# Kernel tuning notes

Measured on AMD Instinct MI355X. Metric: run time of the kernel, lower is better.

The kernel has to match this reference:

```python
import jax, jax.numpy as jnp
import numpy as np

N_NODES = 100000
BN_EPS = 1e-5


def _linear_params(key, fan_in, fan_out):
    k1, k2 = jax.random.split(key)
    lim = 1.0 / np.sqrt(fan_in)
    W = jax.random.uniform(k1, (fan_in, fan_out), jnp.float32, -lim, lim)
    b = jax.random.uniform(k2, (fan_out,), jnp.float32, -lim, lim)
    return W, b


def setup_inputs() -> dict:
    key = jax.random.key(0)
    ks = jax.random.split(key, 24)
    in_ch, hid, tdim, L = 17, 64, 32, 2
    E = 1600000
    inp = {}
    inp["x"] = jax.random.normal(ks[0], (N_NODES, in_ch), jnp.float32)
    inp["edge_index"] = jax.random.randint(ks[1], (2, E), 0, N_NODES, jnp.int64)
    inp["edge_dts"] = jax.random.uniform(ks[2], (E,), jnp.float32) * 100.0
    inp["batch_size"] = 10000
    # TimeEncode params (learned, TGAT init)
    inp["basis_freq"] = jnp.asarray(1.0 / 10 ** np.linspace(0, 9, tdim), jnp.float32)
    inp["phase"] = jnp.zeros((tdim,), jnp.float32)
    # TMP edge MLP: in = 2*in_ch + tdim
    mi = 2 * in_ch + tdim
    inp["tmp_W1"], inp["tmp_b1"] = _linear_params(ks[3], mi, mi // 2)
    inp["tmp_W2"], inp["tmp_b2"] = _linear_params(ks[4], mi // 2, in_ch)
    inp["proj_W"], inp["proj_b"] = _linear_params(ks[5], in_ch, hid)
    # SMP layers (stacked over L)
    si = 2 * hid
    W1s, b1s, W2s, b2s = [], [], [], []
    for l in range(L):
        W1, b1 = _linear_params(ks[6 + 2 * l], si, si // 2)
        W2, b2 = _linear_params(ks[7 + 2 * l], si // 2, hid)
        W1s.append(W1); b1s.append(b1); W2s.append(W2); b2s.append(b2)
    inp["smp_W1"] = jnp.stack(W1s); inp["smp_b1"] = jnp.stack(b1s)
    inp["smp_W2"] = jnp.stack(W2s); inp["smp_b2"] = jnp.stack(b2s)
    inp["bn_gamma"] = jnp.ones((L, hid), jnp.float32)
    inp["bn_beta"] = jnp.zeros((L, hid), jnp.float32)
    # classifier head
    inp["clf_W1"], inp["clf_b1"] = _linear_params(ks[12], hid, hid)
    inp["clf_g1"] = jnp.ones((hid,), jnp.float32); inp["clf_bb1"] = jnp.zeros((hid,), jnp.float32)
    inp["clf_W2"], inp["clf_b2"] = _linear_params(ks[13], hid, hid // 2)
    inp["clf_g2"] = jnp.ones((hid // 2,), jnp.float32); inp["clf_bb2"] = jnp.zeros((hid // 2,), jnp.float32)
    inp["clf_W3"], inp["clf_b3"] = _linear_params(ks[14], hid // 2, 1)
    return inp


def _segment_mean(vals, idx, n):
    s = jax.ops.segment_sum(vals, idx, num_segments=n)
    c = jax.ops.segment_sum(jnp.ones((idx.shape[0], 1), vals.dtype), idx, num_segments=n)
    return s / jnp.maximum(c, 1.0)


def _bn(x, g, b):
    m = x.mean(0)
    v = x.var(0)
    return (x - m) * jax.lax.rsqrt(v + BN_EPS) * g + b


def reference(x, edge_index, edge_dts, batch_size, basis_freq, phase,
              tmp_W1, tmp_b1, tmp_W2, tmp_b2, proj_W, proj_b,
              smp_W1, smp_b1, smp_W2, smp_b2, bn_gamma, bn_beta,
              clf_W1, clf_b1, clf_g1, clf_bb1,
              clf_W2, clf_b2, clf_g2, clf_bb2, clf_W3, clf_b3):
    src, dst = edge_index[0], edge_index[1]  # x_j = x[src], x_i = x[dst]
    n = x.shape[0]
    # TimeEncode: cos(t * freq + phase)  -> [E, time_dim]
    rel = jnp.cos(edge_dts[:, None] * basis_freq + phase)
    # --- TMP conv (applied once) ---
    x_i = x[dst]
    m_in = jnp.concatenate([x_i, x[src], rel], axis=-1)
    p = jnp.tanh(jax.nn.relu(m_in @ tmp_W1 + tmp_b1) @ tmp_W2 + tmp_b2)
    msg = (2.0 * p - 1.0) * x_i  # (p - q) * x_i with q = 1 - p
    h = x + _segment_mean(msg, dst, n)
    # --- project to hidden ---
    h = h @ proj_W + proj_b
    # --- L SMP layers with BatchNorm + ReLU (dropout = eval/identity) ---
    L = smp_W1.shape[0]
    for l in range(L):
        h_i = h[dst]
        m_in = jnp.concatenate([h_i, h[src]], axis=-1)
        p = jnp.tanh(jax.nn.relu(m_in @ smp_W1[l] + smp_b1[l]) @ smp_W2[l] + smp_b2[l])
        h = h + _segment_mean((2.0 * p - 1.0) * h_i, dst, n)
        h = jax.nn.relu(_bn(h, bn_gamma[l], bn_beta[l]))
    # --- classifier on seed nodes ---
    z = h[:batch_size]
    z = jax.nn.relu(_bn(z @ clf_W1 + clf_b1, clf_g1, clf_bb1))
    z = jax.nn.relu(_bn(z @ clf_W2 + clf_b2, clf_g2, clf_bb2))
    return z @ clf_W3 + clf_b3  # [batch_size, 1] logits
```

## Files before the change

### kernel.cpp

```cpp
#include <hip/hip_runtime.h>
#include <hip/hip_bf16.h>


typedef float  f32x4 __attribute__((ext_vector_type(4)));
typedef short  s16x8 __attribute__((ext_vector_type(8)));

__device__ __forceinline__ float tanh_factor(float u) {
  float e = __expf(2.0f * u);
  return fmaf(-4.0f, __builtin_amdgcn_rcpf(e + 1.0f), 1.0f);
}

__device__ __forceinline__ void atomic_add_f32(float* p, float v) {
  unsafeAtomicAdd(p, v);
}

__device__ __forceinline__ unsigned short f2bf(float f) {
  __hip_bfloat16 b = __float2bfloat16(f);
  return *(unsigned short*)&b;
}
__device__ __forceinline__ float bf2f(unsigned short u) {
  unsigned int v = ((unsigned int)u) << 16;
  return *(float*)&v;
}

__global__ __launch_bounds__(256) void k_hist(
    const int* __restrict__ ei, int* __restrict__ cntI, int E)
{
  int e = blockIdx.x * 256 + threadIdx.x;
  if (e < E) atomicAdd(&cntI[__builtin_nontemporal_load(ei + E + e)], 1);
}

__global__ __launch_bounds__(256) void k_scan_block(
    const int* __restrict__ cntI, int* __restrict__ cursor,
    int* __restrict__ bsum, int N)
{
  __shared__ int s[256];
  const int t = threadIdx.x;
  int i = blockIdx.x * 256 + t;
  int v = (i < N) ? cntI[i] : 0;
  s[t] = v;
  for (int off = 1; off < 256; off <<= 1) {
    __syncthreads();
    int x = (t >= off) ? s[t - off] : 0;
    __syncthreads();
    s[t] += x;
  }
  __syncthreads();
  if (i < N) cursor[i] = s[t] - v;
  if (t == 255) bsum[blockIdx.x] = s[255];
}

__global__ __launch_bounds__(512) void k_scan_bsum(int* __restrict__ bsum, int nb)
{
  __shared__ int s[512];
  const int t = threadIdx.x;
  int v = (t < nb) ? bsum[t] : 0;
  s[t] = v;
  for (int off = 1; off < 512; off <<= 1) {
    __syncthreads();
    int x = (t >= off) ? s[t - off] : 0;
    __syncthreads();
    s[t] += x;
  }
  __syncthreads();
  if (t < nb) bsum[t] = s[t] - v;
}

__global__ __launch_bounds__(256) void k_expand_add(
    int* __restrict__ cursor, const int* __restrict__ bsum,
    const int* __restrict__ cntI, int* __restrict__ dstS, int N)
{
  int n = blockIdx.x * 256 + threadIdx.x;
  if (n >= N) return;
  int cur = cursor[n] + bsum[blockIdx.x];
  cursor[n] = cur;
  int c = cntI[n];
  for (int i = 0; i < c; i++) dstS[cur + i] = n;
}

__global__ __launch_bounds__(256) void k_scatter_x(
    const int* __restrict__ ei, const float* __restrict__ dts,
    int* __restrict__ cursor, int2* __restrict__ srcdtS, int E, int N)
{
  const int g  = blockIdx.x & 7;
  const int bi = blockIdx.x >> 3;
  const int nb = gridDim.x >> 3;
  const int lo = (int)(((long long)N * g) >> 3);
  const int hi = (int)(((long long)N * (g + 1)) >> 3);
  for (int e = bi * 256 + threadIdx.x; e < E; e += nb * 256) {
    int d = __builtin_nontemporal_load(ei + E + e);
    if (d >= lo && d < hi) {
      int s = __builtin_nontemporal_load(ei + e);
      float dt = __builtin_nontemporal_load(dts + e);
      int pos = atomicAdd(&cursor[d], 1);
      srcdtS[pos] = make_int2(s, __float_as_int(dt));
    }
  }
}

__global__ __launch_bounds__(256) void prep_all(
    const float* __restrict__ x, const float* __restrict__ tW1,
    const float* __restrict__ tW2, const float* __restrict__ sW1,
    const float* __restrict__ sW2, const float* __restrict__ cW1,
    const float* __restrict__ cW2, unsigned short* __restrict__ xb,
    unsigned short* __restrict__ W1t1, unsigned short* __restrict__ W2t1,
    unsigned short* __restrict__ W1t, unsigned short* __restrict__ W2t,
    unsigned short* __restrict__ cW1t, unsigned short* __restrict__ cW2t,
    float* __restrict__ acc1, float* __restrict__ bnsAll, int N)
{
  int i = blockIdx.x * 256 + threadIdx.x;
  int totalX = N * 24;
  for (int idx = i; idx < totalX; idx += gridDim.x * 256) {
    int n = idx / 24, c = idx - n * 24;
    xb[idx] = (c < 17) ? f2bf(x[n * 17 + c]) : (unsigned short)0;
  }
  for (int idx = i; idx < N * 17; idx += gridDim.x * 256) acc1[idx] = 0.0f;
  if (i < 512) bnsAll[i] = 0.0f;
  if (i < 48 * 96) {
    int n = i / 96, k = i - n * 96;
    int src = (k < 17) ? k : (k >= 24 && k < 41) ? (k - 24 + 17)
            : (k >= 48 && k < 80) ? (k - 48 + 34) : -1;
    W1t1[i] = (n < 33 && src >= 0) ? f2bf(tW1[src * 33 + n]) : (unsigned short)0;
  }
  if (i < 32 * 64) {
    int n = i / 64, k = i - n * 64;
    W2t1[i] = (n < 17 && k < 33) ? f2bf(tW2[k * 17 + n]) : (unsigned short)0;
  }
  if (i < 2 * 64 * 128) {
    int l = i >> 13; int r = i & 8191; int n = r >> 7; int k = r & 127;
    W1t[i] = f2bf(sW1[((size_t)l * 128 + k) * 64 + n]);
  }
  if (i < 2 * 64 * 64) {
    int l = i >> 12; int r = i & 4095; int n = r >> 6; int k = r & 63;
    W2t[i] = f2bf(sW2[((size_t)l * 64 + k) * 64 + n]);
  }
  if (i < 64 * 64) {
    int c = i >> 6, k = i & 63;
    cW1t[i] = f2bf(cW1[k * 64 + c]);
  }
  if (i < 32 * 64) {
    int c = i >> 6, k = i & 63;
    cW2t[i] = f2bf(cW2[k * 32 + c]);
  }
}

__global__ __launch_bounds__(256, 3) void phase1_edge_mfma(
    const unsigned short* __restrict__ xb, const int* __restrict__ dstS,
    const int2* __restrict__ srcdtS, const float* __restrict__ freq,
    const float* __restrict__ phs,
    const unsigned short* __restrict__ W1t1, const float* __restrict__ b1,
    const unsigned short* __restrict__ W2t1, const float* __restrict__ b2,
    float* __restrict__ accum, int E, int nwt)
{
  __shared__ unsigned short sA[64][104];
  __shared__ unsigned short sHid[64][72];
  __shared__ float sRed[64][20];
  __shared__ int   sDst[64];

  const int t = threadIdx.x;
  const int wv = t >> 6, lane = t & 63, l16 = lane & 15, quad = lane >> 4;
  const int r0 = wv * 16;
  const int e_loc = lane >> 2, q = lane & 3;
  const int rr = r0 + e_loc;

  s16x8 w1f[3][3], w2f[2][2];
  float bias1[3], bias2[2];
#pragma unroll
  for (int cb = 0; cb < 3; cb++) {
    int n = cb * 16 + l16;
#pragma unroll
    for (int kb = 0; kb < 3; kb++)
      w1f[cb][kb] = *(const s16x8*)&W1t1[n * 96 + kb * 32 + quad * 8];
    bias1[cb] = (n < 33) ? b1[n] : 0.0f;
  }
#pragma unroll
  for (int cb = 0; cb < 2; cb++) {
    int n = cb * 16 + l16;
#pragma unroll
    for (int kb = 0; kb < 2; kb++)
      w2f[cb][kb] = *(const s16x8*)&W2t1[n * 64 + kb * 32 + quad * 8];
    bias2[cb] = (n < 17) ? b2[n] : 0.0f;
  }

  float frq[8], phv[8];
#pragma unroll
  for (int j = 0; j < 8; j++) {
    frq[j] = freq[q * 8 + j];
    phv[j] = phs[q * 8 + j];
  }

  for (int i = lane; i < 16 * 28; i += 64) {
    int rrz = r0 + i / 28, c = i % 28;
    int col = (c < 6) ? 18 + c : (c < 12) ? 42 + (c - 6) : 80 + (c - 12);
    sA[rrz][col] = 0;
  }
  for (int i = lane; i < 256; i += 64)
    sHid[r0 + (i >> 4)][48 + (i & 15)] = 0;

  const int g8   = blockIdx.x & 7;
  const int tLo  = (int)(((long long)nwt * g8) >> 3);
  const int tHi  = (int)(((long long)nwt * (g8 + 1)) >> 3);
  const int wLoc = (blockIdx.x >> 3) * 4 + wv;
  const int nwLoc = (gridDim.x >> 3) * 4;

  int idxN = 0; float dtN = 0.0f;
  int ndP = 0; uint4 xa0, xa1; unsigned int xa2 = 0; float dtP = 0.0f;
  auto issue_idx = [&](int tt) {
    int er = (tt << 4) + e_loc; if (er >= E) er = E - 1;
    int2 sd = srcdtS[er];
    idxN = q ? sd.x : dstS[er];
    dtN  = __int_as_float(sd.y);
  };
  auto issue_payload = [&]() {
    ndP = idxN; dtP = dtN;
    if (q < 2) {
      const unsigned short* src = &xb[(size_t)ndP * 24];
      xa0 = *(const uint4*)&src[0];
      xa1 = *(const uint4*)&src[8];
      xa2 = *(const unsigned int*)&src[16];
    }
  };
  {
    int t0 = tLo + wLoc; if (t0 >= nwt) t0 = nwt - 1;
    issue_idx(t0);
    issue_payload();
    int t1 = t0 + nwLoc; if (t1 >= tHi) t1 = t0;
    issue_idx(t1);
  }

  for (int tile = tLo + wLoc; tile < tHi; tile += nwLoc) {
    const int eb = tile << 4;

    if (q < 2) {
      if (!q) sDst[rr] = ndP;
      const int base = q ? 24 : 0;
      *(uint4*)&sA[rr][base]     = xa0;
      *(uint4*)&sA[rr][base + 8] = xa1;
      *(unsigned int*)&sA[rr][base + 16] = xa2;
    }
    {
      unsigned short tmp[8] __attribute__((aligned(16)));
#pragma unroll
      for (int j = 0; j < 8; j++)
        tmp[j] = f2bf(__cosf(fmaf(dtP, frq[j], phv[j])));
      *(uint4*)&sA[rr][48 + q * 8] = *(const uint4*)&tmp[0];
    }

    issue_payload();
    { int nt = tile + 2 * nwLoc; issue_idx(nt < tHi ? nt : tile); }

    f32x4 a1[3];
#pragma unroll
    for (int cb = 0; cb < 3; cb++)
      a1[cb] = (f32x4){bias1[cb], bias1[cb], bias1[cb], bias1[cb]};
#pragma unroll
    for (int kb = 0; kb < 3; kb++) {
      s16x8 aF = *(const s16x8*)&sA[r0 + l16][kb * 32 + quad * 8];
#pragma unroll
      for (int cb = 0; cb < 3; cb++)
        a1[cb] = __builtin_amdgcn_mfma_f32_16x16x32_bf16(aF, w1f[cb][kb], a1[cb], 0, 0, 0);
    }
#pragma unroll
    for (int cb = 0; cb < 3; cb++)
#pragma unroll
      for (int reg = 0; reg < 4; reg++)
        sHid[r0 + quad * 4 + reg][cb * 16 + l16] = f2bf(fmaxf(a1[cb][reg], 0.0f));

    f32x4 a2[2];
#pragma unroll
    for (int cb = 0; cb < 2; cb++)
      a2[cb] = (f32x4){bias2[cb], bias2[cb], bias2[cb], bias2[cb]};
#pragma unroll
    for (int kb = 0; kb < 2; kb++) {
      s16x8 aF = *(const s16x8*)&sHid[r0 + l16][kb * 32 + quad * 8];
#pragma unroll
      for (int cb = 0; cb < 2; cb++)
        a2[cb] = __builtin_amdgcn_mfma_f32_16x16x32_bf16(aF, w2f[cb][kb], a2[cb], 0, 0, 0);
    }

#pragma unroll
    for (int reg = 0; reg < 4; reg++) {
      int row = r0 + quad * 4 + reg;
      bool ok = (eb + quad * 4 + reg < E);
      sRed[row][l16] = ok ? tanh_factor(a2[0][reg]) : 0.0f;
      if (l16 == 0) sRed[row][16] = ok ? tanh_factor(a2[1][reg]) : 0.0f;
    }

    if (lane < 17) {
      int col = lane;
      float run = 0.0f;
      int cur = __builtin_amdgcn_readfirstlane(sDst[r0]);
#pragma unroll
      for (int k = 0; k < 16; k++) {
        int d = __builtin_amdgcn_readfirstlane(sDst[r0 + k]);
        float v = sRed[r0 + k][col];
        if (d != cur) {
          atomic_add_f32(&accum[(size_t)cur * 17 + col], run);
          run = 0.0f; cur = d;
        }
        run += v;
      }
      atomic_add_f32(&accum[(size_t)cur * 17 + col], run);
    }
  }
}

__global__ __launch_bounds__(256) void phase1_node(
    const float* __restrict__ x, const float* __restrict__ acc1,
    const int* __restrict__ cntI, const float* __restrict__ Wp,
    const float* __restrict__ bp, float* __restrict__ h,
    float* __restrict__ acc2, int N)
{
  __shared__ float s0[4][20];
  const int t = threadIdx.x;
  const int nb = blockIdx.x << 2;
  if (t < 68) {
    int nl = t / 17, c = t % 17;
    int n = nb + nl;
    float v = 0.0f;
    if (n < N) {
      float cnt = fmaxf((float)cntI[n], 1.0f);
      v = x[n * 17 + c] * (1.0f + acc1[n * 17 + c] / cnt);
    }
    s0[nl][c] = v;
  }
  __syncthreads();
  int nl = t >> 6, j = t & 63;
  int n = nb + nl;
  if (n < N) {
    float acc = bp[j];
#pragma unroll
    for (int c = 0; c < 17; c++) acc = fmaf(s0[nl][c], Wp[c * 64 + j], acc);
    h[n * 64 + j] = acc;
    acc2[n * 64 + j] = 0.0f;
  }
}

template <bool DO_BN>
__global__ void prep_P(
    float* __restrict__ h, const unsigned short* __restrict__ W1t,
    const float* __restrict__ b1,
    const float* __restrict__ bns, const float* __restrict__ bnq,
    const float* __restrict__ gam, const float* __restrict__ bet, float invR,
    unsigned short* __restrict__ P1, unsigned short* __restrict__ P2, int N)
{
  __shared__ unsigned short sH[64][72];
  __shared__ float sM[64], sS[64], sB[64];
  const int t = threadIdx.x;
  const int wv = t >> 6, lane = t & 63, l16 = lane & 15, quad = lane >> 4;
  const int nb = blockIdx.x << 6;

  if (DO_BN) {
    if (t < 64) {
      float m = bns[t] * invR;
      float var = bnq[t] * invR - m * m;
      sM[t] = m;
      sS[t] = gam[t] * rsqrtf(var + 1e-5f);
      sB[t] = bet[t];
    }
    __syncthreads();
  }

#pragma unroll
  for (int i = 0; i < 4; i++) {
    int g = t + i * 256;
    int r = g >> 4, c4 = (g & 15) << 2;
    int n0 = nb + r;
    bool valid = (n0 < N);
    int n = valid ? n0 : N - 1;
    float4 v = *(const float4*)&h[(size_t)n * 64 + c4];
    if (DO_BN) {
      v.x = fmaxf(fmaf(v.x - sM[c4 + 0], sS[c4 + 0], sB[c4 + 0]), 0.0f);
      v.y = fmaxf(fmaf(v.y - sM[c4 + 1], sS[c4 + 1], sB[c4 + 1]), 0.0f);
      v.z = fmaxf(fmaf(v.z - sM[c4 + 2], sS[c4 + 2], sB[c4 + 2]), 0.0f);
      v.w = fmaxf(fmaf(v.w - sM[c4 + 3], sS[c4 + 3], sB[c4 + 3]), 0.0f);
      if (valid) *(float4*)&h[(size_t)n0 * 64 + c4] = v;
    }
    ushort4 o = { f2bf(v.x), f2bf(v.y), f2bf(v.z), f2bf(v.w) };
    *(ushort4*)&sH[r][c4] = o;
  }
  __syncthreads();

  const int n = nb + wv * 16 + l16;
#pragma unroll
  for (int half = 0; half < 2; half++) {
    f32x4 acc[4];
#pragma unroll
    for (int cb = 0; cb < 4; cb++) {
      if (half == 0) {
        float4 bv = *(const float4*)&b1[cb * 16 + quad * 4];
        acc[cb] = (f32x4){bv.x, bv.y, bv.z, bv.w};
      } else {
        acc[cb] = (f32x4){0.0f, 0.0f, 0.0f, 0.0f};
      }
    }
#pragma unroll
    for (int kb = 0; kb < 2; kb++) {
      s16x8 bF = *(const s16x8*)&sH[wv * 16 + l16][kb * 32 + quad * 8];
#pragma unroll
      for (int cb = 0; cb < 4; cb++) {
        s16x8 aF = *(const s16x8*)&W1t[(cb * 16 + l16) * 128 + half * 64 + kb * 32 + quad * 8];
        acc[cb] = __builtin_amdgcn_mfma_f32_16x16x32_bf16(aF, bF, acc[cb], 0, 0, 0);
      }
    }
    if (n < N) {
      unsigned short* P = half ? P2 : P1;
#pragma unroll
      for (int cb = 0; cb < 4; cb++) {
        ushort4 o = { f2bf(acc[cb][0]), f2bf(acc[cb][1]),
                      f2bf(acc[cb][2]), f2bf(acc[cb][3]) };
        *(ushort4*)&P[(size_t)n * 64 + cb * 16 + quad * 4] = o;
      }
    }
  }
}

__global__ __launch_bounds__(256, 5) void phase2_edge(
    const unsigned short* __restrict__ P1, const unsigned short* __restrict__ P2,
    const int* __restrict__ dstS, const int2* __restrict__ srcdtS,
    const unsigned short* __restrict__ W2t, const float* __restrict__ b2,
    float* __restrict__ accum, int E, int nwt)
{
  __shared__ unsigned short sA[64][136];
  __shared__ int sDst[64];
  float* sRedF = (float*)&sA[0][0];

  const int t = threadIdx.x;
  const int wv = t >> 6, lane = t & 63, l16 = lane & 15, quad = lane >> 4;
  const int r0 = wv * 16;

  s16x8 w2f[4][2];
  f32x4 bias2v[4];
#pragma unroll
  for (int cb = 0; cb < 4; cb++) {
#pragma unroll
    for (int kb = 0; kb < 2; kb++)
      w2f[cb][kb] = *(const s16x8*)&W2t[(cb * 16 + l16) * 64 + kb * 32 + quad * 8];
    float4 bv = *(const float4*)&b2[cb * 16 + quad * 4];
    bias2v[cb] = (f32x4){bv.x, bv.y, bv.z, bv.w};
  }

  const int eRow = r0 + l16;

  const int e_loc = lane >> 2, q = lane & 3;
  const int rr = r0 + e_loc;
  const unsigned short* const Pb = (q < 2) ? P1 : P2;
  const int cb0 = q * 32;
  const size_t sub = (size_t)((q & 1) * 32);

  const int g8   = blockIdx.x & 7;
  const int tLo  = (int)(((long long)nwt * g8) >> 3);
  const int tHi  = (int)(((long long)nwt * (g8 + 1)) >> 3);
  const int wLoc = (blockIdx.x >> 3) * 4 + wv;
  const int nwLoc = (gridDim.x >> 3) * 4;

  int idxN = 0;
  int ndP = 0; uint4 pA, pB, pC, pD;
  auto issue_idx = [&](int tt) {
    int er = (tt << 4) + e_loc; if (er >= E) er = E - 1;
    idxN = (q < 2) ? dstS[er] : srcdtS[er].x;
  };
  auto issue_payload = [&]() {
    ndP = idxN;
    const unsigned short* src = Pb + (size_t)ndP * 64 + sub;
    pA = *(const uint4*)&src[0];
    pB = *(const uint4*)&src[8];
    pC = *(const uint4*)&src[16];
    pD = *(const uint4*)&src[24];
  };
  {
    int t0 = tLo + wLoc; if (t0 >= nwt) t0 = nwt - 1;
    issue_idx(t0);
    issue_payload();
    int t1 = t0 + nwLoc; if (t1 >= tHi) t1 = t0;
    issue_idx(t1);
  }

  for (int tile = tLo + wLoc; tile < tHi; tile += nwLoc) {
    const int eb = tile << 4;

    if (q == 0) sDst[rr] = ndP;
    *(uint4*)&sA[rr][cb0]      = pA;
    *(uint4*)&sA[rr][cb0 + 8]  = pB;
    *(uint4*)&sA[rr][cb0 + 16] = pC;
    *(uint4*)&sA[rr][cb0 + 24] = pD;

    issue_payload();
    { int nt = tile + 2 * nwLoc; issue_idx(nt < tHi ? nt : tile); }

    s16x8 hidf[2];
#pragma unroll
    for (int kb = 0; kb < 2; kb++) {
      s16x8 x1 = *(const s16x8*)&sA[eRow][kb * 32 + quad * 8];
      s16x8 x2 = *(const s16x8*)&sA[eRow][64 + kb * 32 + quad * 8];
      s16x8 hf;
#pragma unroll
      for (int j = 0; j < 8; j++) {
        float a = bf2f((unsigned short)x1[j]);
        float b = bf2f((unsigned short)x2[j]);
        hf[j] = (short)f2bf(fmaxf(a + b, 0.0f));
      }
      hidf[kb] = hf;
    }

    f32x4 acc[4];
#pragma unroll
    for (int cb = 0; cb < 4; cb++) acc[cb] = bias2v[cb];
#pragma unroll
    for (int kb = 0; kb < 2; kb++)
#pragma unroll
      for (int cb = 0; cb < 4; cb++)
        acc[cb] = __builtin_amdgcn_mfma_f32_16x16x32_bf16(w2f[cb][kb], hidf[kb], acc[cb], 0, 0, 0);

    bool ok = (eb + l16 < E);
#pragma unroll
    for (int cb = 0; cb < 4; cb++) {
      f32x4 f;
#pragma unroll
      for (int reg = 0; reg < 4; reg++)
        f[reg] = ok ? tanh_factor(acc[cb][reg]) : 0.0f;
      *(f32x4*)&sRedF[eRow * 68 + cb * 16 + quad * 4] = f;
    }

    {
      float run = 0.0f;
      int cur = __builtin_amdgcn_readfirstlane(sDst[r0]);
#pragma unroll
      for (int k = 0; k < 16; k++) {
        int d = __builtin_amdgcn_readfirstlane(sDst[r0 + k]);
        float v = sRedF[(r0 + k) * 68 + lane];
        if (d != cur) {
          atomic_add_f32(&accum[(size_t)cur * 64 + lane], run);
          run = 0.0f; cur = d;
        }
        run += v;
      }
      atomic_add_f32(&accum[(size_t)cur * 64 + lane], run);
    }
  }
}

template <bool ZERO>
__global__ __launch_bounds__(256) void node_update_bn(
    float* __restrict__ h, float* __restrict__ accum,
    const int* __restrict__ cntI, float* __restrict__ bns,
    float* __restrict__ bnq, int N)
{
  const int t = threadIdx.x;
  float ls = 0.0f, lq = 0.0f;
  int total = N * 64;
  for (int idx = blockIdx.x * 256 + t; idx < total; idx += gridDim.x * 256) {
    int n = idx >> 6;
    float cnt = fmaxf((float)cntI[n], 1.0f);
    float v = h[idx] * (1.0f + accum[idx] / cnt);
    if (ZERO) accum[idx] = 0.0f;
    h[idx] = v;
    ls += v; lq += v * v;
  }
  __shared__ float ss[256], sq[256];
  ss[t] = ls; sq[t] = lq;
  __syncthreads();
  if (t < 64) {
    float s = ss[t] + ss[t + 64] + ss[t + 128] + ss[t + 192];
    float q = sq[t] + sq[t + 64] + sq[t + 128] + sq[t + 192];
    atomic_add_f32(&bns[t], s);
    atomic_add_f32(&bnq[t], q);
  }
}

template <int NCB>
__global__ __launch_bounds__(256) void clf_mfma(
    const float* __restrict__ in, const unsigned short* __restrict__ Wt,
    const float* __restrict__ bias, float* __restrict__ z,
    float* __restrict__ bns, float* __restrict__ bnq,
    const float* __restrict__ ibns, const float* __restrict__ ibnq,
    const float* __restrict__ igam, const float* __restrict__ ibet,
    float iinvR, int rows)
{
  __shared__ unsigned short sIn[64][72];
  __shared__ float sM[64], sS[64], sB[64];
  const int t = threadIdx.x;
  const int wv = t >> 6, lane = t & 63, l16 = lane & 15, quad = lane >> 4;
  const int nb = blockIdx.x << 6;

  if (t < 64) {
    float m = ibns[t] * iinvR;
    float var = ibnq[t] * iinvR - m * m;
    sM[t] = m;
    sS[t] = igam[t] * rsqrtf(var + 1e-5f);
    sB[t] = ibet[t];
  }

  s16x8 wf[NCB][2];
  f32x4 bv[NCB];
#pragma unroll
  for (int cb = 0; cb < NCB; cb++) {
#pragma unroll
    for (int kb = 0; kb < 2; kb++)
      wf[cb][kb] = *(const s16x8*)&Wt[(cb * 16 + l16) * 64 + kb * 32 + quad * 8];
    float4 b4 = *(const float4*)&bias[cb * 16 + quad * 4];
    bv[cb] = (f32x4){b4.x, b4.y, b4.z, b4.w};
  }
  __syncthreads();

#pragma unroll
  for (int i = 0; i < 4; i++) {
    int g = t + i * 256;
    int r = g >> 4, c4 = (g & 15) << 2;
    int n = nb + r; if (n >= rows) n = rows - 1;
    float4 v = *(const float4*)&in[(size_t)n * 64 + c4];
    v.x = fmaxf(fmaf(v.x - sM[c4 + 0], sS[c4 + 0], sB[c4 + 0]), 0.0f);
    v.y = fmaxf(fmaf(v.y - sM[c4 + 1], sS[c4 + 1], sB[c4 + 1]), 0.0f);
    v.z = fmaxf(fmaf(v.z - sM[c4 + 2], sS[c4 + 2], sB[c4 + 2]), 0.0f);
    v.w = fmaxf(fmaf(v.w - sM[c4 + 3], sS[c4 + 3], sB[c4 + 3]), 0.0f);
    ushort4 o = { f2bf(v.x), f2bf(v.y), f2bf(v.z), f2bf(v.w) };
    *(ushort4*)&sIn[r][c4] = o;
  }
  __syncthreads();

  const int n = nb + wv * 16 + l16;
  const bool ok = (n < rows);
  f32x4 acc[NCB];
#pragma unroll
  for (int cb = 0; cb < NCB; cb++) acc[cb] = bv[cb];
#pragma unroll
  for (int kb = 0; kb < 2; kb++) {
    s16x8 bF = *(const s16x8*)&sIn[wv * 16 + l16][kb * 32 + quad * 8];
#pragma unroll
    for (int cb = 0; cb < NCB; cb++)
      acc[cb] = __builtin_amdgcn_mfma_f32_16x16x32_bf16(wf[cb][kb], bF, acc[cb], 0, 0, 0);
  }

#pragma unroll
  for (int cb = 0; cb < NCB; cb++) {
    if (ok)
      *(float4*)&z[(size_t)n * (NCB * 16) + cb * 16 + quad * 4] =
          make_float4(acc[cb][0], acc[cb][1], acc[cb][2], acc[cb][3]);
    f32x4 s, q;
#pragma unroll
    for (int reg = 0; reg < 4; reg++) {
      float v = ok ? acc[cb][reg] : 0.0f;
      s[reg] = v; q[reg] = v * v;
    }
#pragma unroll
    for (int m = 1; m < 16; m <<= 1) {
#pragma unroll
      for (int reg = 0; reg < 4; reg++) {
        s[reg] += __shfl_xor(s[reg], m);
        q[reg] += __shfl_xor(q[reg], m);
      }
    }
    if (l16 == 0) {
#pragma unroll
      for (int reg = 0; reg < 4; reg++) {
        int col = cb * 16 + quad * 4 + reg;
        atomic_add_f32(&bns[col], s[reg]);
        atomic_add_f32(&bnq[col], q[reg]);
      }
    }
  }
}

__global__ __launch_bounds__(256) void clf_final(
    const float* __restrict__ z2, const float* __restrict__ W3,
    const float* __restrict__ b3,
    const float* __restrict__ ibns, const float* __restrict__ ibnq,
    const float* __restrict__ igam, const float* __restrict__ ibet,
    float iinvR, float* __restrict__ out, int rows)
{
  __shared__ float sM[32], sS[32], sB[32];
  const int t = threadIdx.x;
  if (t < 32) {
    float m = ibns[t] * iinvR;
    float var = ibnq[t] * iinvR - m * m;
    sM[t] = m;
    sS[t] = igam[t] * rsqrtf(var + 1e-5f);
    sB[t] = ibet[t];
  }
  __syncthreads();
  int n = blockIdx.x * 256 + t;
  if (n >= rows) return;
  float acc = b3[0];
#pragma unroll
  for (int k = 0; k < 32; k++) {
    float v = fmaxf(fmaf(z2[n * 32 + k] - sM[k], sS[k], sB[k]), 0.0f);
    acc = fmaf(v, W3[k], acc);
  }
  out[n] = acc;
}

extern "C" void kernel_launch(void* const* d_in, const int* in_sizes, int n_in,
                              void* d_out, int out_size, void* d_ws, size_t ws_size,
                              hipStream_t stream)
{
  const float* x    = (const float*)d_in[0];
  const int*   ei   = (const int*)  d_in[1];
  const float* dts  = (const float*)d_in[2];
  const float* freq = (const float*)d_in[4];
  const float* phs  = (const float*)d_in[5];
  const float* tW1  = (const float*)d_in[6];
  const float* tb1  = (const float*)d_in[7];
  const float* tW2  = (const float*)d_in[8];
  const float* tb2  = (const float*)d_in[9];
  const float* pW   = (const float*)d_in[10];
  const float* pb   = (const float*)d_in[11];
  const float* sW1  = (const float*)d_in[12];
  const float* sb1  = (const float*)d_in[13];
  const float* sW2  = (const float*)d_in[14];
  const float* sb2  = (const float*)d_in[15];
  const float* bng  = (const float*)d_in[16];
  const float* bnb  = (const float*)d_in[17];
  const float* cW1  = (const float*)d_in[18];
  const float* cb1  = (const float*)d_in[19];
  const float* cg1  = (const float*)d_in[20];
  const float* cbb1 = (const float*)d_in[21];
  const float* cW2  = (const float*)d_in[22];
  const float* cb2  = (const float*)d_in[23];
  const float* cg2  = (const float*)d_in[24];
  const float* cbb2 = (const float*)d_in[25];
  const float* cW3  = (const float*)d_in[26];
  const float* cb3  = (const float*)d_in[27];
  float* out = (float*)d_out;

  const int N = in_sizes[0] / 17;
  const int E = in_sizes[1] / 2;
  const int B = out_size;

  char* base = (char*)d_ws;
  size_t off = 0;
  float* h    = (float*)(base + off); off += (size_t)N * 64 * 4;
  float* acc2 = (float*)(base + off); off += (size_t)N * 64 * 4;
  char*  uni  = base + off;           off += (size_t)N * 64 * 4;
  float* bnsAll = (float*)(base + off); off += 8 * 64 * 4;
  unsigned short* W1t = (unsigned short*)(base + off); off += 2 * 64 * 128 * 2;
  unsigned short* W2t = (unsigned short*)(base + off); off += 2 * 64 * 64 * 2;
  unsigned short* cW1t = (unsigned short*)(base + off); off += 64 * 64 * 2;
  unsigned short* cW2t = (unsigned short*)(base + off); off += 32 * 64 * 2;
  int* cntI   = (int*)(base + off); off += (size_t)N * 4;
  int* cursor = (int*)(base + off); off += (size_t)N * 4;
  int* bsum   = (int*)(base + off); off += 512 * 4;
  int* dstS   = (int*)(base + off); off += (size_t)E * 4;
  off = (off + 15) & ~(size_t)15;
  int2* srcdtS = (int2*)(base + off); off += (size_t)E * 8;
  size_t needed = off;
  if (ws_size < needed) return;

  float* acc1 = (float*)uni;
  unsigned short* xb   = (unsigned short*)(uni + (size_t)N * 17 * 4);
  unsigned short* W1t1 = xb + (size_t)N * 24;
  unsigned short* W2t1 = W1t1 + 48 * 96;
  unsigned short* P1 = (unsigned short*)uni;
  unsigned short* P2 = P1 + (size_t)N * 64;
  float* z1 = (float*)uni;
  float* z2 = z1 + (size_t)B * 64;

  const int nwt = (E + 15) / 16;
  const int NB = (N + 255) / 256;
  if (NB > 512) return;

  hipMemsetAsync(cntI, 0, (size_t)N * 4, stream);

  k_hist<<<(E + 255) / 256, 256, 0, stream>>>(ei, cntI, E);
  k_scan_block<<<NB, 256, 0, stream>>>(cntI, cursor, bsum, N);
  k_scan_bsum<<<1, 512, 0, stream>>>(bsum, NB);
  k_expand_add<<<NB, 256, 0, stream>>>(cursor, bsum, cntI, dstS, N);
  k_scatter_x<<<1024, 256, 0, stream>>>(ei, dts, cursor, srcdtS, E, N);
  prep_all<<<(N * 24 + 255) / 256, 256, 0, stream>>>(
      x, tW1, tW2, sW1, sW2, cW1, cW2, xb, W1t1, W2t1, W1t, W2t,
      cW1t, cW2t, acc1, bnsAll, N);

  phase1_edge_mfma<<<768, 256, 0, stream>>>(
      xb, dstS, srcdtS, freq, phs, W1t1, tb1, W2t1, tb2, acc1, E, nwt);
  phase1_node<<<(N + 3) / 4, 256, 0, stream>>>(x, acc1, cntI, pW, pb, h, acc2, N);

  const int PB = (N + 63) / 64;
  prep_P<false><<<PB, 256, 0, stream>>>(
      h, W1t, sb1, nullptr, nullptr, nullptr, nullptr, 0.0f, P1, P2, N);
  phase2_edge<<<1280, 256, 0, stream>>>(
      P1, P2, dstS, srcdtS, W2t, sb2, acc2, E, nwt);
  node_update_bn<true><<<1024, 256, 0, stream>>>(h, acc2, cntI,
                                                 bnsAll + 0, bnsAll + 64, N);
  prep_P<true><<<PB, 256, 0, stream>>>(
      h, W1t + (size_t)64 * 128, sb1 + 64, bnsAll + 0, bnsAll + 64,
      bng, bnb, 1.0f / (float)N, P1, P2, N);
  phase2_edge<<<1280, 256, 0, stream>>>(
      P1, P2, dstS, srcdtS, W2t + (size_t)64 * 64, sb2 + 64, acc2, E, nwt);
  node_update_bn<false><<<1024, 256, 0, stream>>>(h, acc2, cntI,
                                                  bnsAll + 128, bnsAll + 192, N);

  const int CB = (B + 63) / 64;
  clf_mfma<4><<<CB, 256, 0, stream>>>(
      h, cW1t, cb1, z1, bnsAll + 256, bnsAll + 320,
      bnsAll + 128, bnsAll + 192, bng + 64, bnb + 64, 1.0f / (float)N, B);
  clf_mfma<2><<<CB, 256, 0, stream>>>(
      z1, cW2t, cb2, z2, bnsAll + 384, bnsAll + 448,
      bnsAll + 256, bnsAll + 320, cg1, cbb1, 1.0f / (float)B, B);
  clf_final<<<(B + 255) / 256, 256, 0, stream>>>(
      z2, cW3, cb3, bnsAll + 384, bnsAll + 448, cg2, cbb2,
      1.0f / (float)B, out, B);
}
```

Baseline: 797.3 us.

## Replace 8-pass filtered edge scatter with two-pass bucket partition then scatter

The counting-sort scatter used to make eight passes over the edge list, each group keeping only the edges whose destination fell in one of eight node ranges. Now one vectorized pass partitions edges into eight destination-range buckets, using shared-memory block ranks and one global atomic per bucket per block. A second kernel then scatters each bucket contiguously into the CSR-sorted arrays. This cuts repeated reads of edge_index and dts in exchange for an extra write and read of a temporary bucket array stored in the reused workspace.

```diff
diff --git a/kernel.cpp b/kernel.cpp
--- a/kernel.cpp
+++ b/kernel.cpp
@@ -4,6 +4,7 @@
 
 typedef float  f32x4 __attribute__((ext_vector_type(4)));
 typedef short  s16x8 __attribute__((ext_vector_type(8)));
+typedef int    i32x4 __attribute__((ext_vector_type(4)));
 
 __device__ __forceinline__ float tanh_factor(float u) {
   float e = __expf(2.0f * u);
@@ -68,33 +69,100 @@
 
 __global__ __launch_bounds__(256) void k_expand_add(
     int* __restrict__ cursor, const int* __restrict__ bsum,
-    const int* __restrict__ cntI, int* __restrict__ dstS, int N)
+    const int* __restrict__ cntI, int* __restrict__ dstS,
+    int* __restrict__ bktBase, int* __restrict__ bktCur, int N)
 {
   int n = blockIdx.x * 256 + threadIdx.x;
   if (n >= N) return;
   int cur = cursor[n] + bsum[blockIdx.x];
   cursor[n] = cur;
+#pragma unroll
+  for (int g = 0; g < 8; g++) {
+    int log = (int)(((long long)N * g) >> 3);
+    if (n == log) { bktBase[g] = cur; bktCur[g] = cur; }
+  }
   int c = cntI[n];
   for (int i = 0; i < c; i++) dstS[cur + i] = n;
 }
 
-__global__ __launch_bounds__(256) void k_scatter_x(
+__global__ __launch_bounds__(256) void k_bucket(
     const int* __restrict__ ei, const float* __restrict__ dts,
-    int* __restrict__ cursor, int2* __restrict__ srcdtS, int E, int N)
+    int* __restrict__ bktCur, int* __restrict__ bdst,
+    int2* __restrict__ bsd, int E, int N)
+{
+  __shared__ int lcnt[8], lbase[8];
+  const int t = threadIdx.x;
+  int lo[7];
+#pragma unroll
+  for (int g = 1; g < 8; g++) lo[g - 1] = (int)(((long long)N * g) >> 3);
+
+  const int E4 = (E + 3) >> 2;
+  for (int b4 = blockIdx.x * 256; b4 < E4; b4 += gridDim.x * 256) {
+    int e4 = b4 + t;
+    int d[4], s[4], tv[4], g4[4];
+    bool ok[4];
+    int e0 = e4 << 2;
+    if (e4 < E4 && e0 + 3 < E) {
+      i32x4 dv = __builtin_nontemporal_load((const i32x4*)(ei + E) + e4);
+      i32x4 sv = __builtin_nontemporal_load((const i32x4*)ei + e4);
+      i32x4 tw = __builtin_nontemporal_load((const i32x4*)dts + e4);
+#pragma unroll
+      for (int j = 0; j < 4; j++) {
+        d[j] = dv[j]; s[j] = sv[j]; tv[j] = tw[j]; ok[j] = true;
+      }
+    } else {
+#pragma unroll
+      for (int j = 0; j < 4; j++) {
+        int e = e0 + j;
+        ok[j] = (e4 < E4) && (e < E);
+        d[j]  = ok[j] ? ei[E + e] : 0;
+        s[j]  = ok[j] ? ei[e] : 0;
+        tv[j] = ok[j] ? __float_as_int(dts[e]) : 0;
+      }
+    }
+#pragma unroll
+    for (int j = 0; j < 4; j++) {
+      int g = 0;
+#pragma unroll
+      for (int k = 0; k < 7; k++) g += (d[j] >= lo[k]);
+      g4[j] = g;
+    }
+    if (t < 8) lcnt[t] = 0;
+    __syncthreads();
+    int rank[4];
+#pragma unroll
+    for (int j = 0; j < 4; j++)
+      rank[j] = ok[j] ? atomicAdd(&lcnt[g4[j]], 1) : 0;
+    __syncthreads();
+    if (t < 8) lbase[t] = lcnt[t] ? atomicAdd(&bktCur[t], lcnt[t]) : 0;
+    __syncthreads();
+#pragma unroll
+    for (int j = 0; j < 4; j++) {
+      if (ok[j]) {
+        int pos = lbase[g4[j]] + rank[j];
+        bdst[pos] = d[j];
+        bsd[pos]  = make_int2(s[j], tv[j]);
+      }
+    }
+    __syncthreads();
+  }
+}
+
+__global__ __launch_bounds__(256) void k_scatter2(
+    const int* __restrict__ bktBase, const int* __restrict__ bdst,
+    const int2* __restrict__ bsd, int* __restrict__ cursor,
+    int2* __restrict__ srcdtS, int E)
 {
   const int g  = blockIdx.x & 7;
   const int bi = blockIdx.x >> 3;
   const int nb = gridDim.x >> 3;
-  const int lo = (int)(((long long)N * g) >> 3);
-  const int hi = (int)(((long long)N * (g + 1)) >> 3);
-  for (int e = bi * 256 + threadIdx.x; e < E; e += nb * 256) {
-    int d = __builtin_nontemporal_load(ei + E + e);
-    if (d >= lo && d < hi) {
-      int s = __builtin_nontemporal_load(ei + e);
-      float dt = __builtin_nontemporal_load(dts + e);
-      int pos = atomicAdd(&cursor[d], 1);
-      srcdtS[pos] = make_int2(s, __float_as_int(dt));
-    }
+  const int beg = bktBase[g];
+  const int end = (g < 7) ? bktBase[g + 1] : E;
+  for (int i = beg + bi * 256 + threadIdx.x; i < end; i += nb * 256) {
+    int d   = bdst[i];
+    int2 sd = bsd[i];
+    int pos = atomicAdd(&cursor[d], 1);
+    srcdtS[pos] = sd;
   }
 }
 
@@ -739,6 +807,8 @@
   int* cntI   = (int*)(base + off); off += (size_t)N * 4;
   int* cursor = (int*)(base + off); off += (size_t)N * 4;
   int* bsum   = (int*)(base + off); off += 512 * 4;
+  int* bktBase = (int*)(base + off); off += 8 * 4;
+  int* bktCur  = (int*)(base + off); off += 8 * 4;
   int* dstS   = (int*)(base + off); off += (size_t)E * 4;
   off = (off + 15) & ~(size_t)15;
   int2* srcdtS = (int2*)(base + off); off += (size_t)E * 8;
@@ -753,6 +823,8 @@
   unsigned short* P2 = P1 + (size_t)N * 64;
   float* z1 = (float*)uni;
   float* z2 = z1 + (size_t)B * 64;
+  int*  bdst = (int*)uni;
+  int2* bsd  = (int2*)(uni + (size_t)E * 4);
 
   const int nwt = (E + 15) / 16;
   const int NB = (N + 255) / 256;
@@ -763,8 +835,10 @@
   k_hist<<<(E + 255) / 256, 256, 0, stream>>>(ei, cntI, E);
   k_scan_block<<<NB, 256, 0, stream>>>(cntI, cursor, bsum, N);
   k_scan_bsum<<<1, 512, 0, stream>>>(bsum, NB);
-  k_expand_add<<<NB, 256, 0, stream>>>(cursor, bsum, cntI, dstS, N);
-  k_scatter_x<<<1024, 256, 0, stream>>>(ei, dts, cursor, srcdtS, E, N);
+  k_expand_add<<<NB, 256, 0, stream>>>(cursor, bsum, cntI, dstS,
+                                       bktBase, bktCur, N);
+  k_bucket<<<1024, 256, 0, stream>>>(ei, dts, bktCur, bdst, bsd, E, N);
+  k_scatter2<<<1024, 256, 0, stream>>>(bktBase, bdst, bsd, cursor, srcdtS, E);
   prep_all<<<(N * 24 + 255) / 256, 256, 0, stream>>>(
       x, tW1, tW2, sW1, sW2, cW1, cW2, xb, W1t1, W2t1, W1t, W2t,
       cW1t, cW2t, acc1, bnsAll, N);
```

After: 804.9 us. Within noise of the previous version (+0.9%).
